# Performance work log

Measured on AMD Instinct MI355X. Metric: run time of the kernel, lower is better.

Reference implementation:

```python
import math
import jax, jax.numpy as jnp
import numpy as np

B, P, L, R = 16, 256, 8, 128  # n_embd = L*R = 1024
H = 4 * L * R                 # MLP hidden = 4096

def new_gelu(x):
    # tanh-approx GELU as in NewGELU
    c = math.sqrt(2.0 / math.pi)
    return 0.5 * x * (1.0 + jnp.tanh(c * (x + 0.044715 * x * x * x)))

def setup_inputs() -> dict:
    key = jax.random.key(0)
    k1, k2, k3 = jax.random.split(key, 3)
    x = jax.random.normal(k1, (B, P, L, R), dtype=jnp.float32)
    W1 = jax.random.normal(k2, (L * R, H), dtype=jnp.float32) * 0.02
    b1 = jnp.zeros((H,), dtype=jnp.float32)
    W2 = jax.random.normal(k3, (H, R), dtype=jnp.float32) * 0.02
    b2 = jnp.zeros((R,), dtype=jnp.float32)
    return {"x": x, "W1": W1, "b1": b1, "W2": W2, "b2": b2}

def reference(x, W1, b1, W2, b2):
    b, p, l, r = x.shape
    flat = x.reshape(b, p, l * r)                       # [B,P,L*R]
    # Level i input = flat with first i*R entries zeroed (zeros-pad + tail slice)
    col = jnp.arange(l * r)
    mask = (col[None, :] >= (jnp.arange(l) * r)[:, None]).astype(x.dtype)  # [L, L*R]
    inp = flat[:, :, None, :] * mask                    # [B,P,L,L*R]
    h = new_gelu(jnp.einsum('bple,eh->bplh', inp, W1) + b1)  # [B,P,L,H]
    out = jnp.einsum('bplh,hr->bplr', h, W2) + b2       # [B,P,L,R]
    return out
```

## Files before the change

kernel.cpp:

```cpp
#include <hip/hip_runtime.h>
#include <hip/hip_bf16.h>


typedef _Float16 half8 __attribute__((ext_vector_type(8)));
typedef _Float16 half4 __attribute__((ext_vector_type(4)));
typedef _Float16 half2v __attribute__((ext_vector_type(2)));
typedef float    f32x4  __attribute__((ext_vector_type(4)));
typedef float    f32x16 __attribute__((ext_vector_type(16)));

#define MFMA3216(A,B,C) __builtin_amdgcn_mfma_f32_32x32x16_f16(A, B, C, 0, 0, 0)
#define MFMA1632(A,B,C) __builtin_amdgcn_mfma_f32_16x16x32_f16(A, B, C, 0, 0, 0)

__device__ __forceinline__ float gelu_f(float x){
  float t2 = x * fmaf(x*x, -0.10294324f, -2.30220842f);
  float e  = __builtin_amdgcn_exp2f(t2);
  return x * __builtin_amdgcn_rcpf(1.0f + e);
}

__global__ void k_prep(const float* __restrict__ x, const float* __restrict__ w1,
                       const float* __restrict__ w2,
                       _Float16* __restrict__ xt, _Float16* __restrict__ w1t,
                       _Float16* __restrict__ w2t){
  int bid = blockIdx.x;
  if (bid < 2048){
    int tid = bid*256 + threadIdx.x;
    int lane = tid & 63;
    int kf   = (tid >> 6) & 63;
    int tgg  = tid >> 12;
    int tok = tgg*32 + (lane & 31);
    int k   = kf*16 + (lane >> 5)*8;
    const float4* s4 = reinterpret_cast<const float4*>(x + (size_t)tok*1024 + k);
    float4 a = s4[0], b = s4[1];
    half8 v;
    v[0]=(_Float16)a.x; v[1]=(_Float16)a.y; v[2]=(_Float16)a.z; v[3]=(_Float16)a.w;
    v[4]=(_Float16)b.x; v[5]=(_Float16)b.y; v[6]=(_Float16)b.z; v[7]=(_Float16)b.w;
    *reinterpret_cast<half8*>(xt + (size_t)tid*8) = v;
  } else if (bid < 4096){
    int tid = (bid - 2048)*256 + threadIdx.x;
    int lane = tid & 63;
    int ht   = (tid >> 6) & 15;
    int kf   = (tid >> 10) & 63;
    int hq   = tid >> 16;
    int n = hq*512 + ht*32 + (lane & 31);
    int k = kf*16 + (lane >> 5)*8;
    half8 v;
    #pragma unroll
    for (int jj = 0; jj < 8; ++jj) v[jj] = (_Float16)w1[(size_t)(k + jj)*4096 + n];
    *reinterpret_cast<half8*>(w1t + (size_t)tid*8) = v;
  } else {
    int tid = (bid - 4096)*256 + threadIdx.x;
    int lane = tid & 63;
    int tile = tid >> 6;
    int ntr = tile & 7, kt2 = tile >> 3;
    int n = ntr*16 + (lane & 15);
    int k = kt2*32 + (lane >> 4)*8;
    half8 v;
    #pragma unroll
    for (int jj = 0; jj < 8; ++jj) v[jj] = (_Float16)w2[(size_t)(k + jj)*128 + n];
    *reinterpret_cast<half8*>(w2t + (size_t)tid*8) = v;
  }
}

__global__ void k_init_out(const float* __restrict__ b2, float* __restrict__ out){
  int i = blockIdx.x*256 + threadIdx.x;
  float4 bv = reinterpret_cast<const float4*>(b2)[i & 31];
  reinterpret_cast<float4*>(out)[i] = bv;
}

__global__ void k_reduce(const unsigned* __restrict__ part, const float* __restrict__ b2,
                         float* __restrict__ out){
  int tid = blockIdx.x*256 + threadIdx.x;
  int m16 = tid & 15;
  int rw  = (tid >> 4) & 7;
  int q   = (tid >> 7) & 3;
  int tp  = (tid >> 9) & 1;
  int i   = (tid >> 10) & 3;
  int j   = (tid >> 12) & 7;
  int tt  = tid >> 15;
  float s0 = 0.f, s1 = 0.f;
  #pragma unroll
  for (int hq = 0; hq < 8; ++hq){
    unsigned v = __builtin_nontemporal_load(part + (size_t)hq*2097152 + tid);
    half2v h = __builtin_bit_cast(half2v, v);
    s0 += (float)h[0];
    s1 += (float)h[1];
  }
  int r = rw*16 + m16;
  int tok0 = tt*64 + tp*32 + q*4 + i;
  float bb = b2[r];
  out[(size_t)tok0*1024 + j*128 + r]        = s0 + bb;
  out[(size_t)(tok0 + 16)*1024 + j*128 + r] = s1 + bb;
}

__global__ __launch_bounds__(512, 2) void k_treemlp(
    const _Float16* __restrict__ xt, const _Float16* __restrict__ w1t,
    const _Float16* __restrict__ w2t, const float* __restrict__ b1,
    unsigned* __restrict__ partial, float* __restrict__ out, int use_partial){
  int b    = blockIdx.x;
  int hq   = b & 7;
  int tt   = b >> 3;
  int t    = threadIdx.x;
  int w    = t >> 6;
  int lane = t & 63;
  int t32 = lane & 31, q2 = lane >> 5;
  int m16 = lane & 15, q4 = lane >> 4;

  __shared__ _Float16 Pbuf[32768];
  __shared__ _Float16 Xls[2][8192];

  half8 w2f[16];
  #pragma unroll
  for (int kf = 0; kf < 16; ++kf)
    w2f[kf] = *reinterpret_cast<const half8*>(
        w2t + (size_t)((hq*16 + kf)*8 + w)*512 + lane*8);

  f32x16 acc1[2][2];
  #pragma unroll
  for (int hf = 0; hf < 2; ++hf){
    int base = hq*512 + (w*2 + hf)*32;
    #pragma unroll
    for (int g = 0; g < 4; ++g){
      float4 bv = *reinterpret_cast<const float4*>(b1 + base + 8*g + 4*q2);
      #pragma unroll
      for (int c = 0; c < 4; ++c){
        acc1[hf][0][g*4 + c] = ((const float*)&bv)[c];
        acc1[hf][1][g*4 + c] = ((const float*)&bv)[c];
      }
    }
  }

  #define STAGE_X(J, BUF) do {                                              \
    int s0 = t, s1 = t + 512;                                               \
    half8 v0 = *reinterpret_cast<const half8*>(                             \
        xt + (size_t)((tt*2 + (s0 >> 9))*64 + (J)*8 + ((s0 >> 6) & 7))*512  \
           + (s0 & 63)*8);                                                  \
    half8 v1 = *reinterpret_cast<const half8*>(                             \
        xt + (size_t)((tt*2 + (s1 >> 9))*64 + (J)*8 + ((s1 >> 6) & 7))*512  \
           + (s1 & 63)*8);                                                  \
    *reinterpret_cast<half8*>(&Xls[BUF][s0*8]) = v0;                        \
    *reinterpret_cast<half8*>(&Xls[BUF][s1*8]) = v1;                        \
  } while (0)

  STAGE_X(7, 1);
  __syncthreads();

  const _Float16* w1base = w1t + (size_t)hq*65536*8 + (size_t)(w*2)*512 + lane*8;

  #pragma unroll
  for (int jr = 0; jr < 8; ++jr){
    int j = 7 - jr;
    const _Float16* xb = Xls[j & 1];

    #pragma unroll
    for (int s = 0; s < 8; ++s){
      int kf = j*8 + s;
      half8 a0 = *reinterpret_cast<const half8*>(w1base + (size_t)(kf*16    )*512);
      half8 a1 = *reinterpret_cast<const half8*>(w1base + (size_t)(kf*16 + 1)*512);
      half8 x0 = *reinterpret_cast<const half8*>(xb + ((     s)*64 + lane)*8);
      half8 x1 = *reinterpret_cast<const half8*>(xb + ((8  + s)*64 + lane)*8);
      acc1[0][0] = MFMA3216(a0, x0, acc1[0][0]);
      acc1[0][1] = MFMA3216(a0, x1, acc1[0][1]);
      acc1[1][0] = MFMA3216(a1, x0, acc1[1][0]);
      acc1[1][1] = MFMA3216(a1, x1, acc1[1][1]);
    }

    #pragma unroll
    for (int hf = 0; hf < 2; ++hf){
      int kfp = w*2 + hf;
      #pragma unroll
      for (int tg = 0; tg < 2; ++tg){
        int tf = tg*2 + (t32 >> 4);
        #pragma unroll
        for (int g = 0; g < 4; ++g){
          half4 hv;
          #pragma unroll
          for (int c = 0; c < 4; ++c)
            hv[c] = (_Float16)gelu_f(acc1[hf][tg][g*4 + c]);
          *reinterpret_cast<half4*>(
              Pbuf + ((tf*16 + kfp)*64 + g*16 + (t32 & 15))*8 + 4*q2) = hv;
        }
      }
    }
    __syncthreads();

    if (jr < 7) STAGE_X(j - 1, (j - 1) & 1);

    f32x4 outJ[4];
    #pragma unroll
    for (int tf = 0; tf < 4; ++tf) outJ[tf] = f32x4{0.f, 0.f, 0.f, 0.f};

    #pragma unroll
    for (int kf = 0; kf < 16; ++kf){
      #pragma unroll
      for (int tf = 0; tf < 4; ++tf){
        half8 a2 = *reinterpret_cast<const half8*>(
            Pbuf + ((tf*16 + kf)*64 + lane)*8);
        outJ[tf] = MFMA1632(a2, w2f[kf], outJ[tf]);
      }
    }

    if (use_partial){
      unsigned* pb = partial + (size_t)hq*2097152 + (size_t)tt*32768
                   + (size_t)j*4096 + q4*128 + w*16 + m16;
      #pragma unroll
      for (int i = 0; i < 4; ++i)
        #pragma unroll
        for (int tp = 0; tp < 2; ++tp){
          half2v p;
          p[0] = (_Float16)outJ[tp*2    ][i];
          p[1] = (_Float16)outJ[tp*2 + 1][i];
          __builtin_nontemporal_store(__builtin_bit_cast(unsigned, p),
                                      pb + (size_t)i*1024 + tp*512);
        }
    } else {
      #pragma unroll
      for (int tf = 0; tf < 4; ++tf)
        #pragma unroll
        for (int i = 0; i < 4; ++i){
          int tok = tt*64 + tf*16 + q4*4 + i;
          atomicAdd(out + (size_t)tok*1024 + j*128 + w*16 + m16, outJ[tf][i]);
        }
    }
    __syncthreads();
  }
  #undef STAGE_X
}

extern "C" void kernel_launch(void* const* d_in, const int* in_sizes, int n_in,
                              void* d_out, int out_size, void* d_ws, size_t ws_size,
                              hipStream_t stream){
  (void)in_sizes; (void)n_in; (void)out_size;
  const float* x  = (const float*)d_in[0];
  const float* W1 = (const float*)d_in[1];
  const float* b1 = (const float*)d_in[2];
  const float* W2 = (const float*)d_in[3];
  const float* b2 = (const float*)d_in[4];
  float* out = (float*)d_out;

  _Float16* xt  = (_Float16*)d_ws;
  _Float16* w1t = xt  + 4194304;
  _Float16* w2t = w1t + 4194304;
  unsigned* partial = (unsigned*)(w2t + 524288);
  const size_t need = (size_t)(4194304 + 4194304 + 524288)*2 + (size_t)16777216*4;
  int use_partial = (ws_size >= need) ? 1 : 0;

  hipLaunchKernelGGL(k_prep, dim3(4352), dim3(256), 0, stream, x, W1, W2, xt, w1t, w2t);
  if (!use_partial)
    hipLaunchKernelGGL(k_init_out, dim3(4096), dim3(256), 0, stream, b2, out);
  hipLaunchKernelGGL(k_treemlp, dim3(512), dim3(512), 0, stream,
                     xt, w1t, w2t, b1, partial, out, use_partial);
  if (use_partial)
    hipLaunchKernelGGL(k_reduce, dim3(8192), dim3(256), 0, stream, partial, b2, out);
}
```

Measured before the change: 210.2 us.

## Coalesce x prep through LDS, drop X staging, raise treemlp occupancy

The x conversion in k_prep now runs in 128 blocks that each read a contiguous 32-token chunk into padded shared memory and write MFMA-fragment order out of it, replacing strided per-thread gathers. In k_treemlp the LDS double buffer for X and the register-resident W2 fragments are removed. X and W2 fragments are instead loaded straight from global memory inside the MFMA loops, and launch bounds rise to 4 blocks per CU. This cuts LDS use, register pressure and per-stage barriers to allow more resident waves, at the cost of more global/L2 traffic in the inner loops. k_prep now declares a large static LDS array, which may limit its occupancy for the weight-transpose blocks too.

Result: slower. 228.6 us (+8.7%).

```diff
diff --git a/kernel.cpp b/kernel.cpp
--- a/kernel.cpp
+++ b/kernel.cpp
@@ -17,26 +17,36 @@
   return x * __builtin_amdgcn_rcpf(1.0f + e);
 }
 
+#define XROW 1028
+
 __global__ void k_prep(const float* __restrict__ x, const float* __restrict__ w1,
                        const float* __restrict__ w2,
                        _Float16* __restrict__ xt, _Float16* __restrict__ w1t,
                        _Float16* __restrict__ w2t){
+  __shared__ _Float16 Xs[32*XROW];
   int bid = blockIdx.x;
-  if (bid < 2048){
-    int tid = bid*256 + threadIdx.x;
-    int lane = tid & 63;
-    int kf   = (tid >> 6) & 63;
-    int tgg  = tid >> 12;
-    int tok = tgg*32 + (lane & 31);
-    int k   = kf*16 + (lane >> 5)*8;
-    const float4* s4 = reinterpret_cast<const float4*>(x + (size_t)tok*1024 + k);
-    float4 a = s4[0], b = s4[1];
-    half8 v;
-    v[0]=(_Float16)a.x; v[1]=(_Float16)a.y; v[2]=(_Float16)a.z; v[3]=(_Float16)a.w;
-    v[4]=(_Float16)b.x; v[5]=(_Float16)b.y; v[6]=(_Float16)b.z; v[7]=(_Float16)b.w;
-    *reinterpret_cast<half8*>(xt + (size_t)tid*8) = v;
-  } else if (bid < 4096){
-    int tid = (bid - 2048)*256 + threadIdx.x;
+  int t   = threadIdx.x;
+  if (bid < 128){
+    const float4* x4 = reinterpret_cast<const float4*>(x) + (size_t)bid*8192;
+    #pragma unroll
+    for (int i = 0; i < 32; ++i){
+      float4 v = x4[i*256 + t];
+      half4 h;
+      h[0]=(_Float16)v.x; h[1]=(_Float16)v.y; h[2]=(_Float16)v.z; h[3]=(_Float16)v.w;
+      *reinterpret_cast<half4*>(Xs + i*XROW + t*4) = h;
+    }
+    __syncthreads();
+    #pragma unroll
+    for (int f = 0; f < 16; ++f){
+      int fragidx = f*256 + t;
+      int lane = fragidx & 63, kf = fragidx >> 6;
+      int tok32 = lane & 31;
+      int k = kf*16 + (lane >> 5)*8;
+      half8 v = *reinterpret_cast<const half8*>(Xs + tok32*XROW + k);
+      *reinterpret_cast<half8*>(xt + ((size_t)bid*4096 + fragidx)*8) = v;
+    }
+  } else if (bid < 2176){
+    int tid = (bid - 128)*256 + t;
     int lane = tid & 63;
     int ht   = (tid >> 6) & 15;
     int kf   = (tid >> 10) & 63;
@@ -48,7 +58,7 @@
     for (int jj = 0; jj < 8; ++jj) v[jj] = (_Float16)w1[(size_t)(k + jj)*4096 + n];
     *reinterpret_cast<half8*>(w1t + (size_t)tid*8) = v;
   } else {
-    int tid = (bid - 4096)*256 + threadIdx.x;
+    int tid = (bid - 2176)*256 + t;
     int lane = tid & 63;
     int tile = tid >> 6;
     int ntr = tile & 7, kt2 = tile >> 3;
@@ -92,7 +102,7 @@
   out[(size_t)(tok0 + 16)*1024 + j*128 + r] = s1 + bb;
 }
 
-__global__ __launch_bounds__(512, 2) void k_treemlp(
+__global__ __launch_bounds__(512, 4) void k_treemlp(
     const _Float16* __restrict__ xt, const _Float16* __restrict__ w1t,
     const _Float16* __restrict__ w2t, const float* __restrict__ b1,
     unsigned* __restrict__ partial, float* __restrict__ out, int use_partial){
@@ -106,13 +116,6 @@
   int m16 = lane & 15, q4 = lane >> 4;
 
   __shared__ _Float16 Pbuf[32768];
-  __shared__ _Float16 Xls[2][8192];
-
-  half8 w2f[16];
-  #pragma unroll
-  for (int kf = 0; kf < 16; ++kf)
-    w2f[kf] = *reinterpret_cast<const half8*>(
-        w2t + (size_t)((hq*16 + kf)*8 + w)*512 + lane*8);
 
   f32x16 acc1[2][2];
   #pragma unroll
@@ -129,35 +132,22 @@
     }
   }
 
-  #define STAGE_X(J, BUF) do {                                              \
-    int s0 = t, s1 = t + 512;                                               \
-    half8 v0 = *reinterpret_cast<const half8*>(                             \
-        xt + (size_t)((tt*2 + (s0 >> 9))*64 + (J)*8 + ((s0 >> 6) & 7))*512  \
-           + (s0 & 63)*8);                                                  \
-    half8 v1 = *reinterpret_cast<const half8*>(                             \
-        xt + (size_t)((tt*2 + (s1 >> 9))*64 + (J)*8 + ((s1 >> 6) & 7))*512  \
-           + (s1 & 63)*8);                                                  \
-    *reinterpret_cast<half8*>(&Xls[BUF][s0*8]) = v0;                        \
-    *reinterpret_cast<half8*>(&Xls[BUF][s1*8]) = v1;                        \
-  } while (0)
-
-  STAGE_X(7, 1);
-  __syncthreads();
-
+  const _Float16* xb0 = xt + ((size_t)(tt*2 + 0)*64)*512 + lane*8;
+  const _Float16* xb1 = xt + ((size_t)(tt*2 + 1)*64)*512 + lane*8;
   const _Float16* w1base = w1t + (size_t)hq*65536*8 + (size_t)(w*2)*512 + lane*8;
+  const _Float16* w2base = w2t + (size_t)(hq*16*8 + w)*512 + lane*8;
 
   #pragma unroll
   for (int jr = 0; jr < 8; ++jr){
     int j = 7 - jr;
-    const _Float16* xb = Xls[j & 1];
 
     #pragma unroll
     for (int s = 0; s < 8; ++s){
       int kf = j*8 + s;
       half8 a0 = *reinterpret_cast<const half8*>(w1base + (size_t)(kf*16    )*512);
       half8 a1 = *reinterpret_cast<const half8*>(w1base + (size_t)(kf*16 + 1)*512);
-      half8 x0 = *reinterpret_cast<const half8*>(xb + ((     s)*64 + lane)*8);
-      half8 x1 = *reinterpret_cast<const half8*>(xb + ((8  + s)*64 + lane)*8);
+      half8 x0 = *reinterpret_cast<const half8*>(xb0 + (size_t)kf*512);
+      half8 x1 = *reinterpret_cast<const half8*>(xb1 + (size_t)kf*512);
       acc1[0][0] = MFMA3216(a0, x0, acc1[0][0]);
       acc1[0][1] = MFMA3216(a0, x1, acc1[0][1]);
       acc1[1][0] = MFMA3216(a1, x0, acc1[1][0]);
@@ -183,19 +173,18 @@
     }
     __syncthreads();
 
-    if (jr < 7) STAGE_X(j - 1, (j - 1) & 1);
-
     f32x4 outJ[4];
     #pragma unroll
     for (int tf = 0; tf < 4; ++tf) outJ[tf] = f32x4{0.f, 0.f, 0.f, 0.f};
 
     #pragma unroll
     for (int kf = 0; kf < 16; ++kf){
+      half8 wf = *reinterpret_cast<const half8*>(w2base + (size_t)kf*4096);
       #pragma unroll
       for (int tf = 0; tf < 4; ++tf){
         half8 a2 = *reinterpret_cast<const half8*>(
             Pbuf + ((tf*16 + kf)*64 + lane)*8);
-        outJ[tf] = MFMA1632(a2, w2f[kf], outJ[tf]);
+        outJ[tf] = MFMA1632(a2, wf, outJ[tf]);
       }
     }
 
@@ -223,7 +212,6 @@
     }
     __syncthreads();
   }
-  #undef STAGE_X
 }
 
 extern "C" void kernel_launch(void* const* d_in, const int* in_sizes, int n_in,
@@ -244,7 +232,7 @@
   const size_t need = (size_t)(4194304 + 4194304 + 524288)*2 + (size_t)16777216*4;
   int use_partial = (ws_size >= need) ? 1 : 0;
 
-  hipLaunchKernelGGL(k_prep, dim3(4352), dim3(256), 0, stream, x, W1, W2, xt, w1t, w2t);
+  hipLaunchKernelGGL(k_prep, dim3(2432), dim3(256), 0, stream, x, W1, W2, xt, w1t, w2t);
   if (!use_partial)
     hipLaunchKernelGGL(k_init_out, dim3(4096), dim3(256), 0, stream, b2, out);
   hipLaunchKernelGGL(k_treemlp, dim3(512), dim3(512), 0, stream,
```
